# Performance work log

Hardware: AMD Instinct MI355X
Metric: run time of the kernel (lower is better)

The kernel has to match this reference:

```python
import jax, jax.numpy as jnp
import numpy as np
from jax import lax

EPS = 1e-5

def _bn(x, g, b, m, v):
    # eval-mode BatchNorm2d over channel dim of NCHW
    return (x - m[None, :, None, None]) * (g / jnp.sqrt(v + EPS))[None, :, None, None] + b[None, :, None, None]


def _forward(x, proj_w, proj_b, bn0_g, bn0_b, bn0_m, bn0_v,
             in_proj_w, conv_w, conv_b, x_proj_w, dt_w, dt_b, A_log, D,
             out_proj_w, fc_w, fc_b,
             c1_w, c1_b, bn1_g, bn1_b, bn1_m, bn1_v,
             c2_w, c2_b, bn2_g, bn2_b, bn2_m, bn2_v):
    d_state = A_log.shape[1]
    # ---- spectral projection: 1x1 conv + BN + ReLU ----
    p = jnp.einsum('bchw,dc->bdhw', x, proj_w) + proj_b[None, :, None, None]
    p = jax.nn.relu(_bn(p, bn0_g, bn0_b, bn0_m, bn0_v))
    b, d, h, w = p.shape
    L = h * w
    tok = p.reshape(b, d, L).transpose(0, 2, 1)            # [b, L, d_model]

    # ---- Mamba block (d_model=32, d_state=16, d_conv=4, expand=2) ----
    xz = tok @ in_proj_w.T                                 # [b, L, 2*d_in]
    d_in = xz.shape[-1] // 2
    xm, z = xz[..., :d_in], xz[..., d_in:]
    # causal depthwise conv1d along sequence
    xc = lax.conv_general_dilated(
        xm.transpose(0, 2, 1), conv_w[:, None, :], (1,),
        [(conv_w.shape[-1] - 1, 0)], feature_group_count=d_in,
        dimension_numbers=('NCH', 'OIH', 'NCH'))
    u = jax.nn.silu(xc + conv_b[None, :, None]).transpose(0, 2, 1)  # [b, L, d_in]
    xdbl = u @ x_proj_w.T                                  # [b, L, dt_rank+2N]
    dt_rank = dt_w.shape[1]
    dt = xdbl[..., :dt_rank]
    Bm = xdbl[..., dt_rank:dt_rank + d_state]              # [b, L, N]
    Cm = xdbl[..., dt_rank + d_state:]                     # [b, L, N]
    delta = jax.nn.softplus(dt @ dt_w.T + dt_b)            # [b, L, d_in]
    A = -jnp.exp(A_log)                                    # [d_in, N]

    def step(hst, inp):
        d_t, B_t, C_t, u_t = inp                           # [b,d_in],[b,N],[b,N],[b,d_in]
        dA = jnp.exp(d_t[..., None] * A)                   # [b, d_in, N]
        hst = dA * hst + (d_t * u_t)[..., None] * B_t[:, None, :]
        y_t = jnp.einsum('bdn,bn->bd', hst, C_t)
        return hst, y_t

    h0 = jnp.zeros((b, d_in, d_state), dtype=u.dtype)
    xs = (delta.transpose(1, 0, 2), Bm.transpose(1, 0, 2),
          Cm.transpose(1, 0, 2), u.transpose(1, 0, 2))
    _, ys = lax.scan(step, h0, xs)                         # [L, b, d_in]
    y = ys.transpose(1, 0, 2) + u * D                      # D skip
    y = y * jax.nn.silu(z)                                 # gated
    m_out = y @ out_proj_w.T                               # [b, L, d_model]
    mamba_feat = (m_out @ fc_w.T + fc_b).mean(axis=1)      # [b, FEATURE_DIM]

    # ---- CNN branch ----
    dn = ('NCHW', 'OIHW', 'NCHW')
    c = lax.conv_general_dilated(p, c1_w, (1, 1), 'VALID', dimension_numbers=dn) + c1_b[None, :, None, None]
    c = jax.nn.relu(_bn(c, bn1_g, bn1_b, bn1_m, bn1_v))
    c = lax.conv_general_dilated(c, c2_w, (1, 1), 'VALID', dimension_numbers=dn) + c2_b[None, :, None, None]
    c = jax.nn.relu(_bn(c, bn2_g, bn2_b, bn2_m, bn2_v))
    cnn_feat = c.mean(axis=(2, 3))                         # AdaptiveAvgPool2d(1)+Flatten
    return mamba_feat + cnn_feat


def setup_inputs() -> dict:
    key = jax.random.key(0)
    ks = jax.random.split(key, 16)
    B, C_IN, P = 128, 200, 32
    D_MODEL, D_IN, N, DTR, FDIM = 32, 64, 16, 2, 128
    r = lambda k, s, sc=0.05: jax.random.normal(k, s, jnp.float32) * sc
    f32 = jnp.float32
    return {
        'x': jax.random.normal(ks[0], (B, C_IN, P, P), f32),
        'proj_w': r(ks[1], (D_MODEL, C_IN)),
        'proj_b': jnp.zeros((D_MODEL,), f32),
        'bn0_g': jnp.ones((D_MODEL,), f32), 'bn0_b': jnp.zeros((D_MODEL,), f32),
        'bn0_m': jnp.zeros((D_MODEL,), f32), 'bn0_v': jnp.ones((D_MODEL,), f32),
        'in_proj_w': r(ks[2], (2 * D_IN, D_MODEL)),
        'conv_w': r(ks[3], (D_IN, 4), 0.3),
        'conv_b': jnp.zeros((D_IN,), f32),
        'x_proj_w': r(ks[4], (DTR + 2 * N, D_IN)),
        'dt_w': r(ks[5], (D_IN, DTR), 0.5),
        'dt_b': r(ks[6], (D_IN,), 0.5) - 4.0,
        'A_log': jnp.tile(jnp.log(jnp.arange(1, N + 1, dtype=f32))[None, :], (D_IN, 1)),
        'D': jnp.ones((D_IN,), f32),
        'out_proj_w': r(ks[7], (D_MODEL, D_IN)),
        'fc_w': r(ks[8], (FDIM, D_MODEL)),
        'fc_b': jnp.zeros((FDIM,), f32),
        'c1_w': r(ks[9], (32, D_MODEL, 3, 3)),
        'c1_b': jnp.zeros((32,), f32),
        'bn1_g': jnp.ones((32,), f32), 'bn1_b': jnp.zeros((32,), f32),
        'bn1_m': jnp.zeros((32,), f32), 'bn1_v': jnp.ones((32,), f32),
        'c2_w': r(ks[10], (FDIM, 32, 3, 3)),
        'c2_b': jnp.zeros((FDIM,), f32),
        'bn2_g': jnp.ones((FDIM,), f32), 'bn2_b': jnp.zeros((FDIM,), f32),
        'bn2_m': jnp.zeros((FDIM,), f32), 'bn2_v': jnp.ones((FDIM,), f32),
    }


def reference(x, proj_w, proj_b, bn0_g, bn0_b, bn0_m, bn0_v,
              in_proj_w, conv_w, conv_b, x_proj_w, dt_w, dt_b, A_log, D,
              out_proj_w, fc_w, fc_b,
              c1_w, c1_b, bn1_g, bn1_b, bn1_m, bn1_v,
              c2_w, c2_b, bn2_g, bn2_b, bn2_m, bn2_v):
    return _forward(x, proj_w, proj_b, bn0_g, bn0_b, bn0_m, bn0_v,
                    in_proj_w, conv_w, conv_b, x_proj_w, dt_w, dt_b, A_log, D,
                    out_proj_w, fc_w, fc_b,
                    c1_w, c1_b, bn1_g, bn1_b, bn1_m, bn1_v,
                    c2_w, c2_b, bn2_g, bn2_b, bn2_m, bn2_v)
```

## Files before the change

kernel.cpp:

```cpp
#include <hip/hip_runtime.h>
#include <cstdint>

typedef short bf16x8 __attribute__((ext_vector_type(8)));
typedef float f32x4 __attribute__((ext_vector_type(4)));
#define MFMA16(a, b, c) __builtin_amdgcn_mfma_f32_16x16x32_bf16((a), (b), (c), 0, 0, 0)

static __device__ __forceinline__ float fastrcp(float x) {
  float r;
  asm("v_rcp_f32 %0, %1" : "=v"(r) : "v"(x));
  return r;
}
static __device__ __forceinline__ float fastexp2(float x) {
  float r;
  asm("v_exp_f32 %0, %1" : "=v"(r) : "v"(x));
  return r;
}
static __device__ __forceinline__ float silu_(float x) {
  return x * fastrcp(1.f + __expf(-x));
}
static __device__ __forceinline__ unsigned short f2bf(float f) {
  union { float f; unsigned u; } v; v.f = f;
  unsigned r = v.u + 0x7FFF + ((v.u >> 16) & 1);
  return (unsigned short)(r >> 16);
}
static __device__ __forceinline__ void bf2x(unsigned p, float& lo, float& hi) {
  union { unsigned u; float f; } a, bb;
  a.u = p << 16; bb.u = p & 0xffff0000u;
  lo = a.f; hi = bb.f;
}
static __device__ __forceinline__ float bflo(unsigned short h) {
  union { unsigned u; float f; } a;
  a.u = ((unsigned)h) << 16;
  return a.f;
}

__global__ __launch_bounds__(256, 4) void k_front(
    const float* __restrict__ x, const float* __restrict__ pw,
    const float* __restrict__ pb,
    const float* __restrict__ g0, const float* __restrict__ be0,
    const float* __restrict__ mm0, const float* __restrict__ vv0,
    const float* __restrict__ c1_w, const float* __restrict__ c2_w,
    const float* __restrict__ fc_w, const float* __restrict__ opw,
    const float* __restrict__ in_w, const float* __restrict__ xp_w,
    unsigned short* __restrict__ p_bf,
    unsigned short* __restrict__ Wf1, unsigned short* __restrict__ Wf2,
    unsigned short* __restrict__ Wfin, unsigned short* __restrict__ Wfxp,
    float* __restrict__ W2, float* __restrict__ cnn_sum)
{
  __shared__ __align__(16) char fsm[55296];
  int tid = threadIdx.x;
  if (blockIdx.x >= 512) {
    int i = (blockIdx.x - 512) * 256 + tid;
    if (i < 36864) {
      int j = i & 7, l = (i >> 3) & 63, m = (i >> 9) & 7, t = i >> 12;
      int co = m * 16 + (l & 15), ci = ((l >> 4) << 3) + j;
      Wf2[i] = f2bf(c2_w[(size_t)(co * 32 + ci) * 9 + t]);
    } else if (i < 46080) {
      int ii = i - 36864;
      int j = ii & 7, l = (ii >> 3) & 63, m = (ii >> 9) & 1, t = ii >> 10;
      int co = m * 16 + (l & 15), ci = ((l >> 4) << 3) + j;
      Wf1[ii] = f2bf(c1_w[(size_t)(co * 32 + ci) * 9 + t]);
    } else if (i < 54272) {
      int ii = i - 46080;
      int f = ii >> 6, d2 = ii & 63;
      float a = 0.f;
      #pragma unroll
      for (int dm = 0; dm < 32; dm++) a = fmaf(fc_w[(f << 5) + dm], opw[(dm << 6) + d2], a);
      W2[ii] = a;
    } else if (i < 70656) {
      cnn_sum[i - 54272] = 0.f;
    } else if (i < 74752) {
      int ii = i - 70656;
      int j = ii & 7, l = (ii >> 3) & 63, ot = ii >> 9;
      int o = (ot << 4) + (l & 15), c = ((l >> 4) << 3) + j;
      Wfin[ii] = f2bf(in_w[(o << 5) + c]);
    } else if (i < 77824) {
      int ii = i - 74752;
      int j = ii & 7, l = (ii >> 3) & 63, kh = (ii >> 9) & 1, ot = ii >> 10;
      int jr = (ot << 4) + (l & 15), c = (kh << 5) + ((l >> 4) << 3) + j;
      Wfxp[ii] = (jr < 34) ? f2bf(xp_w[(jr << 6) + c]) : (unsigned short)0;
    }
    return;
  }
  unsigned* xT = (unsigned*)fsm;
  unsigned short* WfpL = (unsigned short*)(fsm + 40960);
  int b = blockIdx.x >> 2, l0 = (blockIdx.x & 3) << 8;
  int lane = tid & 63, w = tid >> 6;
  int li = lane & 15, kg4 = (lane >> 4) << 2;
  for (int i = tid; i < 7168; i += 256) {
    int j = i & 7, l = (i >> 3) & 63, m = (i >> 9) & 1, kt = i >> 10;
    int co = (m << 4) + (l & 15), c = (kt << 5) + ((l >> 4) << 3) + j;
    WfpL[i] = (c < 200) ? f2bf(pw[co * 200 + c]) : (unsigned short)0;
  }
  float scv[2][4], sbv[2][4];
  #pragma unroll
  for (int m = 0; m < 2; m++)
    #pragma unroll
    for (int jj = 0; jj < 4; jj++) {
      int co = m * 16 + ((lane >> 4) << 2) + jj;
      float s = g0[co] * rsqrtf(vv0[co] + 1e-5f);
      scv[m][jj] = s;
      sbv[m][jj] = fmaf(pb[co] - mm0[co], s, be0[co]);
    }
  const float* xb = x + (size_t)b * 200 * 1024 + l0 + tid;
  #pragma unroll
  for (int p = 0; p < 16; p++) {
    float v0 = xb[(2 * p) << 10];
    float v1 = xb[(2 * p + 1) << 10];
    xT[tid * 20 + p] = (unsigned)f2bf(v0) | ((unsigned)f2bf(v1) << 16);
  }
  __syncthreads();
  f32x4 acc[4][2];
  #pragma unroll
  for (int q = 0; q < 4; q++) {
    acc[q][0] = (f32x4){0.f, 0.f, 0.f, 0.f};
    acc[q][1] = (f32x4){0.f, 0.f, 0.f, 0.f};
  }
  int buf = 0;
  for (int kt = 0; kt < 7; kt++) {
    if (kt < 6) {
      const float* xc = xb + (((size_t)(kt + 1)) << 15);
      int cb = (kt + 1) * 32;
      #pragma unroll
      for (int p = 0; p < 16; p++) {
        int c = cb + 2 * p;
        float v0 = (c < 200) ? xc[(2 * p) << 10] : 0.f;
        float v1 = (c + 1 < 200) ? xc[(2 * p + 1) << 10] : 0.f;
        xT[(buf ^ 1) * 5120 + tid * 20 + p] = (unsigned)f2bf(v0) | ((unsigned)f2bf(v1) << 16);
      }
    }
    bf16x8 a0 = *reinterpret_cast<const bf16x8*>(&WfpL[(((kt << 1) + 0) * 64 + lane) << 3]);
    bf16x8 a1 = *reinterpret_cast<const bf16x8*>(&WfpL[(((kt << 1) + 1) * 64 + lane) << 3]);
    #pragma unroll
    for (int q = 0; q < 4; q++) {
      int px = ((w + (q << 2)) << 4) + li;
      bf16x8 bfr = *reinterpret_cast<const bf16x8*>(&xT[buf * 5120 + px * 20 + kg4]);
      acc[q][0] = MFMA16(a0, bfr, acc[q][0]);
      acc[q][1] = MFMA16(a1, bfr, acc[q][1]);
    }
    __syncthreads();
    buf ^= 1;
  }
  #pragma unroll
  for (int q = 0; q < 4; q++) {
    int px = ((w + (q << 2)) << 4) + li;
    size_t obase = (((size_t)b << 10) + l0 + px) << 5;
    #pragma unroll
    for (int m = 0; m < 2; m++) {
      f32x4 av = acc[q][m];
      ushort4 pk;
      pk.x = f2bf(fmaxf(fmaf(av[0], scv[m][0], sbv[m][0]), 0.f));
      pk.y = f2bf(fmaxf(fmaf(av[1], scv[m][1], sbv[m][1]), 0.f));
      pk.z = f2bf(fmaxf(fmaf(av[2], scv[m][2], sbv[m][2]), 0.f));
      pk.w = f2bf(fmaxf(fmaf(av[3], scv[m][3], sbv[m][3]), 0.f));
      *reinterpret_cast<ushort4*>(&p_bf[obase + m * 16 + ((lane >> 4) << 2)]) = pk;
    }
  }
}

__global__ __launch_bounds__(1024, 4) void k_mamba(
    const unsigned short* __restrict__ p_bf,
    const unsigned short* __restrict__ Wfin,
    const unsigned short* __restrict__ Wfxp,
    const float* __restrict__ conv_w,
    const float* __restrict__ conv_b,
    const float* __restrict__ dt_w,
    const float* __restrict__ dt_b,
    const float* __restrict__ A_log,
    float* __restrict__ pqrs,
    float* __restrict__ au_g)
{
  __shared__ __align__(16) char smem[65072];
  float* xm  = (float*)smem;
  float* dlS = (float*)smem;
  unsigned short* ubS  = (unsigned short*)(smem + 18224);
  unsigned short* uTb  = (unsigned short*)(smem + 27440);
  unsigned short* duzP = (unsigned short*)(smem + 36656);
  float* bcT  = (float*)(smem + 54064);
  float* cwS  = (float*)(smem + 62768);
  float* cbS  = (float*)(smem + 63792);
  float* dtwS = (float*)(smem + 64048);
  float* dtbS = (float*)(smem + 64560);
  float* auS  = (float*)(smem + 64816);

  int b = blockIdx.x >> 4, ch = blockIdx.x & 15;
  int tid = threadIdx.x, lane = tid & 63, w = tid >> 6;
  int li = lane & 15, cig8 = (lane >> 4) << 3;

  if (tid < 256) cwS[tid] = conv_w[tid];
  else if (tid < 320) cbS[tid - 256] = conv_b[tid - 256];
  else if (tid < 448) dtwS[tid - 320] = dt_w[tid - 320];
  else if (tid < 512) dtbS[tid - 448] = dt_b[tid - 448];
  else if (tid < 576) auS[tid - 512] = 0.f;

  const unsigned short* pbf_b = p_bf + ((size_t)b << 15);

  for (int j = w; j < 36; j += 16) {
    if (j < 20) {
      int ot = j / 5, tt = j % 5;
      int r = tt * 16 + li;
      int tg = (ch << 6) + r - 3;
      bf16x8 bfr = {0,0,0,0,0,0,0,0};
      if (r < 67 && tg >= 0)
        bfr = *reinterpret_cast<const bf16x8*>(pbf_b + ((size_t)tg << 5) + cig8);
      bf16x8 aW = *reinterpret_cast<const bf16x8*>(&Wfin[((ot << 6) + lane) << 3]);
      f32x4 acc = {0.f, 0.f, 0.f, 0.f};
      acc = MFMA16(aW, bfr, acc);
      if (r < 67)
        *reinterpret_cast<float4*>(&xm[r * 68 + (ot << 4) + ((lane >> 4) << 2)]) =
            make_float4(acc[0], acc[1], acc[2], acc[3]);
    } else {
      int jz = j - 20;
      int zot = jz >> 2, tt = jz & 3;
      int t = tt * 16 + li;
      int tg = (ch << 6) + t;
      bf16x8 bfr = *reinterpret_cast<const bf16x8*>(pbf_b + ((size_t)tg << 5) + cig8);
      bf16x8 aW = *reinterpret_cast<const bf16x8*>(&Wfin[(((4 + zot) << 6) + lane) << 3]);
      f32x4 acc = {0.f, 0.f, 0.f, 0.f};
      acc = MFMA16(aW, bfr, acc);
      int dzb = (zot << 4) + ((lane >> 4) << 2);
      int toff = ((t >> 2) << 3) + 4 + (t & 3);
      #pragma unroll
      for (int q = 0; q < 4; q++)
        duzP[(dzb + q) * 136 + toff] = f2bf(silu_(acc[q]));
    }
  }
  __syncthreads();
  {
    int d2 = tid & 63, oct = tid >> 6;
    int t0 = oct << 2;
    float4 cw4 = *reinterpret_cast<const float4*>(&cwS[d2 << 2]);
    float cb1 = cbS[d2];
    float x0 = xm[t0 * 68 + d2], x1 = xm[(t0 + 1) * 68 + d2], x2 = xm[(t0 + 2) * 68 + d2];
    uint2 zz2 = *reinterpret_cast<const uint2*>(&duzP[d2 * 136 + (oct << 3) + 4]);
    float zf[4];
    bf2x(zz2.x, zf[0], zf[1]); bf2x(zz2.y, zf[2], zf[3]);
    unsigned short up[4];
    float aup = 0.f;
    #pragma unroll
    for (int s = 0; s < 4; s++) {
      int t = t0 + s;
      float x3 = xm[(t + 3) * 68 + d2];
      float a = cb1;
      a = fmaf(cw4.x, x0, a); a = fmaf(cw4.y, x1, a);
      a = fmaf(cw4.z, x2, a); a = fmaf(cw4.w, x3, a);
      float uu = silu_(a);
      unsigned short ub_ = f2bf(uu);
      ubS[t * 72 + d2] = ub_;
      up[s] = ub_;
      aup = fmaf(uu, zf[s], aup);
      x0 = x1; x1 = x2; x2 = x3;
    }
    uint2 pk;
    pk.x = (unsigned)up[0] | ((unsigned)up[1] << 16);
    pk.y = (unsigned)up[2] | ((unsigned)up[3] << 16);
    *reinterpret_cast<uint2*>(&uTb[d2 * 72 + t0]) = pk;
    atomicAdd(&auS[d2], aup);
  }
  __syncthreads();
  if (w < 12) {
    int ot = w >> 2, tt = w & 3;
    int t = tt * 16 + li;
    const unsigned short* ub = &ubS[t * 72];
    bf16x8 b0 = *reinterpret_cast<const bf16x8*>(ub + cig8);
    bf16x8 b1 = *reinterpret_cast<const bf16x8*>(ub + 32 + cig8);
    bf16x8 a0 = *reinterpret_cast<const bf16x8*>(&Wfxp[(((ot << 1) + 0) * 64 + lane) << 3]);
    bf16x8 a1 = *reinterpret_cast<const bf16x8*>(&Wfxp[(((ot << 1) + 1) * 64 + lane) << 3]);
    f32x4 acc = {0.f, 0.f, 0.f, 0.f};
    acc = MFMA16(a0, b0, acc);
    acc = MFMA16(a1, b1, acc);
    int jb = (ot << 4) + ((lane >> 4) << 2);
    #pragma unroll
    for (int q = 0; q < 4; q++) {
      int jj = jb + q;
      if (jj < 2) bcT[(t & 31) * 68 + 64 + (jj << 1) + (t >> 5)] = acc[q];
      else if (jj < 34) bcT[(jj - 2) * 68 + t] = acc[q];
    }
  }
  __syncthreads();
  {
    int t = tid >> 4, dq = (tid & 15) << 2;
    int tr = t & 31, th = t >> 5;
    float d0 = bcT[tr * 68 + 64 + th];
    float d1 = bcT[tr * 68 + 66 + th];
    int toff = ((t >> 2) << 3) + (t & 3);
    #pragma unroll
    for (int q = 0; q < 4; q++) {
      int dg = dq + q;
      float pre = fmaf(d0, dtwS[dg << 1], fmaf(d1, dtwS[(dg << 1) + 1], dtbS[dg]));
      float dl_ = (pre > 20.f) ? pre : __logf(1.f + __expf(pre));
      dlS[dg * 68 + t] = dl_;
      float uf = bflo(uTb[dg * 72 + t]);
      duzP[dg * 136 + toff] = f2bf(dl_ * uf);
    }
  }
  __syncthreads();
  {
    int sd = tid >> 4, sn = tid & 15;
    float Areg2 = -__expf(A_log[(sd << 4) + sn]) * 1.44269504f;
    float P = 1.f, qq = 0.f, R = 0.f, S = 0.f;
    const float* dr = &dlS[sd * 68];
    const unsigned short* dz = &duzP[sd * 136];
    const float* Br = &bcT[sn * 68];
    const float* Cr = &bcT[(16 + sn) * 68];
    float4 dv = *reinterpret_cast<const float4*>(dr);
    uint4 duz = *reinterpret_cast<const uint4*>(dz);
    float4 Bv = *reinterpret_cast<const float4*>(Br);
    float4 Cv = *reinterpret_cast<const float4*>(Cr);
    for (int g = 0; g < 16; g++) {
      float4 dvc = dv; uint4 dzc = duz; float4 Bvc = Bv; float4 Cvc = Cv;
      if (g < 15) {
        dv  = *reinterpret_cast<const float4*>(dr + ((g + 1) << 2));
        duz = *reinterpret_cast<const uint4*>(dz + ((g + 1) << 3));
        Bv  = *reinterpret_cast<const float4*>(Br + ((g + 1) << 2));
        Cv  = *reinterpret_cast<const float4*>(Cr + ((g + 1) << 2));
      }
      float du0, du1, du2, du3, z0, z1, z2, z3;
      bf2x(dzc.x, du0, du1); bf2x(dzc.y, du2, du3);
      bf2x(dzc.z, z0, z1);  bf2x(dzc.w, z2, z3);
      float e0 = fastexp2(dvc.x * Areg2), e1 = fastexp2(dvc.y * Areg2);
      float e2 = fastexp2(dvc.z * Areg2), e3 = fastexp2(dvc.w * Areg2);
      float c0 = Cvc.x * z0, c1 = Cvc.y * z1, c2 = Cvc.z * z2, c3 = Cvc.w * z3;
      P = e0 * P; qq = fmaf(e0, qq, du0 * Bvc.x); R = fmaf(c0, P, R); S = fmaf(c0, qq, S);
      P = e1 * P; qq = fmaf(e1, qq, du1 * Bvc.y); R = fmaf(c1, P, R); S = fmaf(c1, qq, S);
      P = e2 * P; qq = fmaf(e2, qq, du2 * Bvc.z); R = fmaf(c2, P, R); S = fmaf(c2, qq, S);
      P = e3 * P; qq = fmaf(e3, qq, du3 * Bvc.w); R = fmaf(c3, P, R); S = fmaf(c3, qq, S);
    }
    size_t idx = ((((size_t)b << 4) + ch) << 10) + (sd << 4) + sn;
    *reinterpret_cast<float4*>(pqrs + (idx << 2)) = make_float4(P, qq, R, S);
    if (sn == 0) au_g[((((size_t)b << 4) + ch) << 6) + sd] = auS[sd];
  }
}

__global__ __launch_bounds__(256) void k_conv1m(
    const unsigned short* __restrict__ p_bf, const unsigned short* __restrict__ Wf1,
    const float* __restrict__ cbias,
    const float* __restrict__ g, const float* __restrict__ be,
    const float* __restrict__ mm, const float* __restrict__ vv,
    unsigned short* __restrict__ c1_bf)
{
  __shared__ __align__(16) unsigned short inS[8 * 32 * 40];
  int b = blockIdx.x / 5, s = blockIdx.x % 5;
  int y0 = s * 6;
  int tid = threadIdx.x, lane = tid & 63, w = tid >> 6;
  int li = lane & 15, cig8 = (lane >> 4) << 3;
  for (int uu = tid; uu < 1024; uu += 256) {
    int r = uu >> 7, rem = uu & 127;
    uint4 v = *reinterpret_cast<const uint4*>(
        &p_bf[((((size_t)b << 10) + (y0 + r) * 32) << 5) + rem * 8]);
    int xx = rem >> 2, cg = rem & 3;
    *reinterpret_cast<uint4*>(&inS[(r * 32 + xx) * 40 + cg * 8]) = v;
  }
  bf16x8 aw[9][2];
  #pragma unroll
  for (int t = 0; t < 9; t++)
    #pragma unroll
    for (int m = 0; m < 2; m++)
      aw[t][m] = *reinterpret_cast<const bf16x8*>(&Wf1[(((t << 1) + m) * 64 + lane) * 8]);
  float scv[2][4], sbv[2][4];
  #pragma unroll
  for (int m = 0; m < 2; m++)
    #pragma unroll
    for (int j = 0; j < 4; j++) {
      int co = m * 16 + ((lane >> 4) << 2) + j;
      float sc = g[co] * rsqrtf(vv[co] + 1e-5f);
      scv[m][j] = sc;
      sbv[m][j] = fmaf(cbias[co] - mm[co], sc, be[co]);
    }
  __syncthreads();
  #pragma unroll
  for (int q = 0; q < 3; q++) {
    int pf = w + q * 4;
    int p = pf * 16 + li;
    int pv = (p < 180) ? p : 0;
    int ry = pv / 30, rx = pv % 30;
    f32x4 a0 = {0.f, 0.f, 0.f, 0.f}, a1 = {0.f, 0.f, 0.f, 0.f};
    #pragma unroll
    for (int t = 0; t < 9; t++) {
      int dy = t / 3, dx = t % 3;
      bf16x8 bfr = *reinterpret_cast<const bf16x8*>(
          &inS[((ry + dy) * 32 + rx + dx) * 40 + cig8]);
      a0 = MFMA16(aw[t][0], bfr, a0);
      a1 = MFMA16(aw[t][1], bfr, a1);
    }
    if (p < 180) {
      size_t obase = ((size_t)b * 900 + (size_t)(y0 + ry) * 30 + rx) << 5;
      #pragma unroll
      for (int m = 0; m < 2; m++) {
        f32x4 av = m ? a1 : a0;
        ushort4 pk;
        pk.x = f2bf(fmaxf(fmaf(av[0], scv[m][0], sbv[m][0]), 0.f));
        pk.y = f2bf(fmaxf(fmaf(av[1], scv[m][1], sbv[m][1]), 0.f));
        pk.z = f2bf(fmaxf(fmaf(av[2], scv[m][2], sbv[m][2]), 0.f));
        pk.w = f2bf(fmaxf(fmaf(av[3], scv[m][3], sbv[m][3]), 0.f));
        *reinterpret_cast<ushort4*>(&c1_bf[obase + m * 16 + ((lane >> 4) << 2)]) = pk;
      }
    }
  }
}

__global__ __launch_bounds__(256) void k_back(
    const unsigned short* __restrict__ c1_bf, const unsigned short* __restrict__ Wf2,
    const float* __restrict__ cb2,
    const float* __restrict__ g, const float* __restrict__ be,
    const float* __restrict__ mm, const float* __restrict__ vv,
    const float* __restrict__ pqrs, const float* __restrict__ au_g,
    const float* __restrict__ Dp,
    float* __restrict__ cnn_sum, float* __restrict__ ybar)
{
  __shared__ __align__(16) unsigned short inS[6 * 30 * 40];
  int tid = threadIdx.x;
  if (blockIdx.x >= 896) {
    int cb = blockIdx.x - 896;
    int b = cb >> 2, qq4 = cb & 3;
    int sd = (qq4 << 4) + (tid >> 4), sn = tid & 15;
    float4 pq[16];
    #pragma unroll
    for (int c = 0; c < 16; c++) {
      size_t idx = ((((size_t)b << 4) + c) << 10) + (sd << 4) + sn;
      pq[c] = *reinterpret_cast<const float4*>(pqrs + (idx << 2));
    }
    float h = 0.f, y = 0.f;
    #pragma unroll
    for (int c = 0; c < 16; c++) {
      y = fmaf(pq[c].z, h, y + pq[c].w);
      h = fmaf(pq[c].x, h, pq[c].y);
    }
    float val = y + Dp[sd] * au_g[((((size_t)b << 4) + sn) << 6) + sd];
    val += __shfl_xor(val, 1); val += __shfl_xor(val, 2);
    val += __shfl_xor(val, 4); val += __shfl_xor(val, 8);
    if (sn == 0) ybar[(b << 6) + sd] = val * (1.f / 1024.f);
    return;
  }
  int b = blockIdx.x / 7, s = blockIdx.x % 7;
  int y0 = s * 4;
  int lane = tid & 63, w = tid >> 6;
  int li = lane & 15, cig8 = (lane >> 4) << 3;
  for (int uu = tid; uu < 720; uu += 256) {
    int r = uu / 120, rem = uu % 120;
    uint4 v = *reinterpret_cast<const uint4*>(
        &c1_bf[(((size_t)b * 900 + (size_t)(y0 + r) * 30) << 5) + rem * 8]);
    int xx = rem >> 2, cg = rem & 3;
    *reinterpret_cast<uint4*>(&inS[(r * 30 + xx) * 40 + cg * 8]) = v;
  }
  bf16x8 aw[9][2];
  #pragma unroll
  for (int t = 0; t < 9; t++)
    #pragma unroll
    for (int m = 0; m < 2; m++)
      aw[t][m] = *reinterpret_cast<const bf16x8*>(&Wf2[(((t << 3) + (w << 1) + m) * 64 + lane) * 8]);
  float scv[2][4], sbv[2][4];
  float psum[2][4] = {{0.f,0.f,0.f,0.f},{0.f,0.f,0.f,0.f}};
  #pragma unroll
  for (int m = 0; m < 2; m++)
    #pragma unroll
    for (int j = 0; j < 4; j++) {
      int co = (w << 5) + m * 16 + ((lane >> 4) << 2) + j;
      float sc = g[co] * rsqrtf(vv[co] + 1e-5f);
      scv[m][j] = sc;
      sbv[m][j] = fmaf(cb2[co] - mm[co], sc, be[co]);
    }
  __syncthreads();
  #pragma unroll
  for (int pf = 0; pf < 7; pf++) {
    int p = pf * 16 + li;
    int ry = p / 28, rx = p % 28;
    f32x4 a0 = {0.f, 0.f, 0.f, 0.f}, a1 = {0.f, 0.f, 0.f, 0.f};
    #pragma unroll
    for (int t = 0; t < 9; t++) {
      int dy = t / 3, dx = t % 3;
      bf16x8 bfr = *reinterpret_cast<const bf16x8*>(
          &inS[((ry + dy) * 30 + rx + dx) * 40 + cig8]);
      a0 = MFMA16(aw[t][0], bfr, a0);
      a1 = MFMA16(aw[t][1], bfr, a1);
    }
    #pragma unroll
    for (int j = 0; j < 4; j++) {
      psum[0][j] += fmaxf(fmaf(a0[j], scv[0][j], sbv[0][j]), 0.f);
      psum[1][j] += fmaxf(fmaf(a1[j], scv[1][j], sbv[1][j]), 0.f);
    }
  }
  #pragma unroll
  for (int m = 0; m < 2; m++)
    #pragma unroll
    for (int j = 0; j < 4; j++) {
      float v = psum[m][j];
      v += __shfl_xor(v, 1); v += __shfl_xor(v, 2);
      v += __shfl_xor(v, 4); v += __shfl_xor(v, 8);
      if (li == 0) {
        int co = (w << 5) + m * 16 + ((lane >> 4) << 2) + j;
        atomicAdd(&cnn_sum[((size_t)b << 7) + co], v);
      }
    }
}

__global__ __launch_bounds__(256) void k_final(
    const float* __restrict__ ybar, const float* __restrict__ W2,
    const float* __restrict__ fc_b, const float* __restrict__ cnn_sum,
    float* __restrict__ out)
{
  int i = blockIdx.x * 256 + threadIdx.x;
  int b = i >> 7, f = i & 127;
  float a = 0.f;
  #pragma unroll
  for (int d2 = 0; d2 < 64; d2++) a = fmaf(ybar[(b << 6) + d2], W2[(f << 6) + d2], a);
  out[i] = a + fc_b[f] + cnn_sum[i] * (1.f / 784.f);
}

extern "C" void kernel_launch(void* const* d_in, const int* in_sizes, int n_in,
                              void* d_out, int out_size, void* d_ws, size_t ws_size,
                              hipStream_t stream) {
  (void)in_sizes; (void)n_in; (void)out_size; (void)ws_size;
  const float* x         = (const float*)d_in[0];
  const float* proj_w    = (const float*)d_in[1];
  const float* proj_b    = (const float*)d_in[2];
  const float* bn0_g     = (const float*)d_in[3];
  const float* bn0_b     = (const float*)d_in[4];
  const float* bn0_m     = (const float*)d_in[5];
  const float* bn0_v     = (const float*)d_in[6];
  const float* in_proj_w = (const float*)d_in[7];
  const float* conv_w    = (const float*)d_in[8];
  const float* conv_b    = (const float*)d_in[9];
  const float* x_proj_w  = (const float*)d_in[10];
  const float* dt_w      = (const float*)d_in[11];
  const float* dt_b      = (const float*)d_in[12];
  const float* A_log     = (const float*)d_in[13];
  const float* Dp        = (const float*)d_in[14];
  const float* out_proj_w= (const float*)d_in[15];
  const float* fc_w      = (const float*)d_in[16];
  const float* fc_b      = (const float*)d_in[17];
  const float* c1_w      = (const float*)d_in[18];
  const float* c1_b      = (const float*)d_in[19];
  const float* bn1_g     = (const float*)d_in[20];
  const float* bn1_b     = (const float*)d_in[21];
  const float* bn1_m     = (const float*)d_in[22];
  const float* bn1_v     = (const float*)d_in[23];
  const float* c2_w      = (const float*)d_in[24];
  const float* c2_b      = (const float*)d_in[25];
  const float* bn2_g     = (const float*)d_in[26];
  const float* bn2_b     = (const float*)d_in[27];
  const float* bn2_m     = (const float*)d_in[28];
  const float* bn2_v     = (const float*)d_in[29];
  float* out = (float*)d_out;
  float* ws  = (float*)d_ws;
  float* ybar    = ws;
  float* cnn_sum = ws + 8192;
  float* W2      = ws + 24576;
  float* pqrs    = ws + 32768;
  float* au_g    = ws + 8421376;
  unsigned short* p_bf  = (unsigned short*)(ws + 8552448);
  unsigned short* c1_bf = (unsigned short*)(ws + 10649600);
  unsigned short* Wf1   = (unsigned short*)(ws + 12492800);
  unsigned short* Wf2   = (unsigned short*)(ws + 12497408);
  unsigned short* Wfin  = (unsigned short*)(ws + 12515840);
  unsigned short* Wfxp  = (unsigned short*)(ws + 12517888);

  k_front<<<dim3(816), dim3(256), 0, stream>>>(x, proj_w, proj_b, bn0_g, bn0_b, bn0_m, bn0_v,
                                               c1_w, c2_w, fc_w, out_proj_w, in_proj_w, x_proj_w,
                                               p_bf, Wf1, Wf2, Wfin, Wfxp, W2, cnn_sum);
  k_mamba<<<dim3(2048), dim3(1024), 0, stream>>>(p_bf, Wfin, Wfxp, conv_w, conv_b, dt_w, dt_b,
                                                 A_log, pqrs, au_g);
  k_conv1m<<<dim3(640), dim3(256), 0, stream>>>(p_bf, Wf1, c1_b, bn1_g, bn1_b, bn1_m, bn1_v, c1_bf);
  k_back<<<dim3(1408), dim3(256), 0, stream>>>(c1_bf, Wf2, c2_b, bn2_g, bn2_b, bn2_m, bn2_v,
                                               pqrs, au_g, Dp, cnn_sum, ybar);
  k_final<<<dim3(64), dim3(256), 0, stream>>>(ybar, W2, fc_b, cnn_sum, out);
}
```

Before: 129.8 us.

## Fold conv1 into mamba launch and restructure conv2 to per-wave global loads

Removes the separate conv1 kernel by giving its work to the first 160 blocks of the mamba launch, where each wave computes a slice directly from global memory without LDS staging. The conv2 part of k_back is regrouped into 1024-thread blocks, with each wave loading inputs and weights from global or cache instead of staging through shared memory and registers. The scan loop drops its manual register prefetch, and the dt/softplus thread mapping changes. Launch bounds go up to 8 waves per SIMD, which may force register spills. Without LDS reuse, conv loads are repeated per tap, and the conv1 blocks hold the full 65 KB shared allocation even though they do not use it.

```diff
diff --git a/kernel.cpp b/kernel.cpp
--- a/kernel.cpp
+++ b/kernel.cpp
@@ -158,7 +158,7 @@
   }
 }
 
-__global__ __launch_bounds__(1024, 4) void k_mamba(
+__global__ __launch_bounds__(1024, 8) void k_mamba(
     const unsigned short* __restrict__ p_bf,
     const unsigned short* __restrict__ Wfin,
     const unsigned short* __restrict__ Wfxp,
@@ -167,10 +167,67 @@
     const float* __restrict__ dt_w,
     const float* __restrict__ dt_b,
     const float* __restrict__ A_log,
+    const unsigned short* __restrict__ Wf1,
+    const float* __restrict__ c1bias,
+    const float* __restrict__ g1, const float* __restrict__ be1,
+    const float* __restrict__ mm1, const float* __restrict__ vv1,
+    unsigned short* __restrict__ c1_bf,
     float* __restrict__ pqrs,
     float* __restrict__ au_g)
 {
   __shared__ __align__(16) char smem[65072];
+  int tid = threadIdx.x, lane = tid & 63, w = tid >> 6;
+  int li = lane & 15, cig8 = (lane >> 4) << 3;
+
+  if (blockIdx.x < 160) {
+    int j = blockIdx.x * 16 + w;
+    int ob = j >> 2, ow = j & 3;
+    int b1 = ob / 5, s1 = ob % 5;
+    int y0 = s1 * 6;
+    float scv[2][4], sbv[2][4];
+    #pragma unroll
+    for (int m = 0; m < 2; m++)
+      #pragma unroll
+      for (int jj = 0; jj < 4; jj++) {
+        int co = m * 16 + ((lane >> 4) << 2) + jj;
+        float sc = g1[co] * rsqrtf(vv1[co] + 1e-5f);
+        scv[m][jj] = sc;
+        sbv[m][jj] = fmaf(c1bias[co] - mm1[co], sc, be1[co]);
+      }
+    #pragma unroll
+    for (int q = 0; q < 3; q++) {
+      int pf = ow + (q << 2);
+      int p = pf * 16 + li;
+      int pv = (p < 180) ? p : 0;
+      int ry = pv / 30, rx = pv % 30;
+      f32x4 a0 = {0.f, 0.f, 0.f, 0.f}, a1 = {0.f, 0.f, 0.f, 0.f};
+      #pragma unroll
+      for (int t = 0; t < 9; t++) {
+        int dy = t / 3, dx = t % 3;
+        bf16x8 bfr = *reinterpret_cast<const bf16x8*>(
+            &p_bf[((((size_t)b1 << 10) + (y0 + ry + dy) * 32 + rx + dx) << 5) + cig8]);
+        bf16x8 w0 = *reinterpret_cast<const bf16x8*>(&Wf1[(((t << 1) + 0) * 64 + lane) << 3]);
+        bf16x8 w1 = *reinterpret_cast<const bf16x8*>(&Wf1[(((t << 1) + 1) * 64 + lane) << 3]);
+        a0 = MFMA16(w0, bfr, a0);
+        a1 = MFMA16(w1, bfr, a1);
+      }
+      if (p < 180) {
+        size_t obase = ((size_t)b1 * 900 + (size_t)(y0 + ry) * 30 + rx) << 5;
+        #pragma unroll
+        for (int m = 0; m < 2; m++) {
+          f32x4 av = m ? a1 : a0;
+          ushort4 pk;
+          pk.x = f2bf(fmaxf(fmaf(av[0], scv[m][0], sbv[m][0]), 0.f));
+          pk.y = f2bf(fmaxf(fmaf(av[1], scv[m][1], sbv[m][1]), 0.f));
+          pk.z = f2bf(fmaxf(fmaf(av[2], scv[m][2], sbv[m][2]), 0.f));
+          pk.w = f2bf(fmaxf(fmaf(av[3], scv[m][3], sbv[m][3]), 0.f));
+          *reinterpret_cast<ushort4*>(&c1_bf[obase + m * 16 + ((lane >> 4) << 2)]) = pk;
+        }
+      }
+    }
+    return;
+  }
+
   float* xm  = (float*)smem;
   float* dlS = (float*)smem;
   unsigned short* ubS  = (unsigned short*)(smem + 18224);
@@ -183,9 +240,8 @@
   float* dtbS = (float*)(smem + 64560);
   float* auS  = (float*)(smem + 64816);
 
-  int b = blockIdx.x >> 4, ch = blockIdx.x & 15;
-  int tid = threadIdx.x, lane = tid & 63, w = tid >> 6;
-  int li = lane & 15, cig8 = (lane >> 4) << 3;
+  int bm = blockIdx.x - 160;
+  int b = bm >> 4, ch = bm & 15;
 
   if (tid < 256) cwS[tid] = conv_w[tid];
   else if (tid < 320) cbS[tid - 256] = conv_b[tid - 256];
@@ -279,14 +335,14 @@
   }
   __syncthreads();
   {
-    int t = tid >> 4, dq = (tid & 15) << 2;
+    int t = tid >> 4, l15 = tid & 15;
     int tr = t & 31, th = t >> 5;
     float d0 = bcT[tr * 68 + 64 + th];
     float d1 = bcT[tr * 68 + 66 + th];
     int toff = ((t >> 2) << 3) + (t & 3);
     #pragma unroll
     for (int q = 0; q < 4; q++) {
-      int dg = dq + q;
+      int dg = l15 + (q << 4);
       float pre = fmaf(d0, dtwS[dg << 1], fmaf(d1, dtwS[(dg << 1) + 1], dtbS[dg]));
       float dl_ = (pre > 20.f) ? pre : __logf(1.f + __expf(pre));
       dlS[dg * 68 + t] = dl_;
@@ -303,28 +359,21 @@
     const unsigned short* dz = &duzP[sd * 136];
     const float* Br = &bcT[sn * 68];
     const float* Cr = &bcT[(16 + sn) * 68];
-    float4 dv = *reinterpret_cast<const float4*>(dr);
-    uint4 duz = *reinterpret_cast<const uint4*>(dz);
-    float4 Bv = *reinterpret_cast<const float4*>(Br);
-    float4 Cv = *reinterpret_cast<const float4*>(Cr);
     for (int g = 0; g < 16; g++) {
-      float4 dvc = dv; uint4 dzc = duz; float4 Bvc = Bv; float4 Cvc = Cv;
-      if (g < 15) {
-        dv  = *reinterpret_cast<const float4*>(dr + ((g + 1) << 2));
-        duz = *reinterpret_cast<const uint4*>(dz + ((g + 1) << 3));
-        Bv  = *reinterpret_cast<const float4*>(Br + ((g + 1) << 2));
-        Cv  = *reinterpret_cast<const float4*>(Cr + ((g + 1) << 2));
-      }
+      float4 dv = *reinterpret_cast<const float4*>(dr + (g << 2));
+      uint4 duz = *reinterpret_cast<const uint4*>(dz + (g << 3));
+      float4 Bv = *reinterpret_cast<const float4*>(Br + (g << 2));
+      float4 Cv = *reinterpret_cast<const float4*>(Cr + (g << 2));
       float du0, du1, du2, du3, z0, z1, z2, z3;
-      bf2x(dzc.x, du0, du1); bf2x(dzc.y, du2, du3);
-      bf2x(dzc.z, z0, z1);  bf2x(dzc.w, z2, z3);
-      float e0 = fastexp2(dvc.x * Areg2), e1 = fastexp2(dvc.y * Areg2);
-      float e2 = fastexp2(dvc.z * Areg2), e3 = fastexp2(dvc.w * Areg2);
-      float c0 = Cvc.x * z0, c1 = Cvc.y * z1, c2 = Cvc.z * z2, c3 = Cvc.w * z3;
-      P = e0 * P; qq = fmaf(e0, qq, du0 * Bvc.x); R = fmaf(c0, P, R); S = fmaf(c0, qq, S);
-      P = e1 * P; qq = fmaf(e1, qq, du1 * Bvc.y); R = fmaf(c1, P, R); S = fmaf(c1, qq, S);
-      P = e2 * P; qq = fmaf(e2, qq, du2 * Bvc.z); R = fmaf(c2, P, R); S = fmaf(c2, qq, S);
-      P = e3 * P; qq = fmaf(e3, qq, du3 * Bvc.w); R = fmaf(c3, P, R); S = fmaf(c3, qq, S);
+      bf2x(duz.x, du0, du1); bf2x(duz.y, du2, du3);
+      bf2x(duz.z, z0, z1);  bf2x(duz.w, z2, z3);
+      float e0 = fastexp2(dv.x * Areg2), e1 = fastexp2(dv.y * Areg2);
+      float e2 = fastexp2(dv.z * Areg2), e3 = fastexp2(dv.w * Areg2);
+      float c0 = Cv.x * z0, c1 = Cv.y * z1, c2 = Cv.z * z2, c3 = Cv.w * z3;
+      P = e0 * P; qq = fmaf(e0, qq, du0 * Bv.x); R = fmaf(c0, P, R); S = fmaf(c0, qq, S);
+      P = e1 * P; qq = fmaf(e1, qq, du1 * Bv.y); R = fmaf(c1, P, R); S = fmaf(c1, qq, S);
+      P = e2 * P; qq = fmaf(e2, qq, du2 * Bv.z); R = fmaf(c2, P, R); S = fmaf(c2, qq, S);
+      P = e3 * P; qq = fmaf(e3, qq, du3 * Bv.w); R = fmaf(c3, P, R); S = fmaf(c3, qq, S);
     }
     size_t idx = ((((size_t)b << 4) + ch) << 10) + (sd << 4) + sn;
     *reinterpret_cast<float4*>(pqrs + (idx << 2)) = make_float4(P, qq, R, S);
@@ -332,74 +381,7 @@
   }
 }
 
-__global__ __launch_bounds__(256) void k_conv1m(
-    const unsigned short* __restrict__ p_bf, const unsigned short* __restrict__ Wf1,
-    const float* __restrict__ cbias,
-    const float* __restrict__ g, const float* __restrict__ be,
-    const float* __restrict__ mm, const float* __restrict__ vv,
-    unsigned short* __restrict__ c1_bf)
-{
-  __shared__ __align__(16) unsigned short inS[8 * 32 * 40];
-  int b = blockIdx.x / 5, s = blockIdx.x % 5;
-  int y0 = s * 6;
-  int tid = threadIdx.x, lane = tid & 63, w = tid >> 6;
-  int li = lane & 15, cig8 = (lane >> 4) << 3;
-  for (int uu = tid; uu < 1024; uu += 256) {
-    int r = uu >> 7, rem = uu & 127;
-    uint4 v = *reinterpret_cast<const uint4*>(
-        &p_bf[((((size_t)b << 10) + (y0 + r) * 32) << 5) + rem * 8]);
-    int xx = rem >> 2, cg = rem & 3;
-    *reinterpret_cast<uint4*>(&inS[(r * 32 + xx) * 40 + cg * 8]) = v;
-  }
-  bf16x8 aw[9][2];
-  #pragma unroll
-  for (int t = 0; t < 9; t++)
-    #pragma unroll
-    for (int m = 0; m < 2; m++)
-      aw[t][m] = *reinterpret_cast<const bf16x8*>(&Wf1[(((t << 1) + m) * 64 + lane) * 8]);
-  float scv[2][4], sbv[2][4];
-  #pragma unroll
-  for (int m = 0; m < 2; m++)
-    #pragma unroll
-    for (int j = 0; j < 4; j++) {
-      int co = m * 16 + ((lane >> 4) << 2) + j;
-      float sc = g[co] * rsqrtf(vv[co] + 1e-5f);
-      scv[m][j] = sc;
-      sbv[m][j] = fmaf(cbias[co] - mm[co], sc, be[co]);
-    }
-  __syncthreads();
-  #pragma unroll
-  for (int q = 0; q < 3; q++) {
-    int pf = w + q * 4;
-    int p = pf * 16 + li;
-    int pv = (p < 180) ? p : 0;
-    int ry = pv / 30, rx = pv % 30;
-    f32x4 a0 = {0.f, 0.f, 0.f, 0.f}, a1 = {0.f, 0.f, 0.f, 0.f};
-    #pragma unroll
-    for (int t = 0; t < 9; t++) {
-      int dy = t / 3, dx = t % 3;
-      bf16x8 bfr = *reinterpret_cast<const bf16x8*>(
-          &inS[((ry + dy) * 32 + rx + dx) * 40 + cig8]);
-      a0 = MFMA16(aw[t][0], bfr, a0);
-      a1 = MFMA16(aw[t][1], bfr, a1);
-    }
-    if (p < 180) {
-      size_t obase = ((size_t)b * 900 + (size_t)(y0 + ry) * 30 + rx) << 5;
-      #pragma unroll
-      for (int m = 0; m < 2; m++) {
-        f32x4 av = m ? a1 : a0;
-        ushort4 pk;
-        pk.x = f2bf(fmaxf(fmaf(av[0], scv[m][0], sbv[m][0]), 0.f));
-        pk.y = f2bf(fmaxf(fmaf(av[1], scv[m][1], sbv[m][1]), 0.f));
-        pk.z = f2bf(fmaxf(fmaf(av[2], scv[m][2], sbv[m][2]), 0.f));
-        pk.w = f2bf(fmaxf(fmaf(av[3], scv[m][3], sbv[m][3]), 0.f));
-        *reinterpret_cast<ushort4*>(&c1_bf[obase + m * 16 + ((lane >> 4) << 2)]) = pk;
-      }
-    }
-  }
-}
-
-__global__ __launch_bounds__(256) void k_back(
+__global__ __launch_bounds__(1024, 8) void k_back(
     const unsigned short* __restrict__ c1_bf, const unsigned short* __restrict__ Wf2,
     const float* __restrict__ cb2,
     const float* __restrict__ g, const float* __restrict__ be,
@@ -408,23 +390,24 @@
     const float* __restrict__ Dp,
     float* __restrict__ cnn_sum, float* __restrict__ ybar)
 {
-  __shared__ __align__(16) unsigned short inS[6 * 30 * 40];
-  int tid = threadIdx.x;
-  if (blockIdx.x >= 896) {
-    int cb = blockIdx.x - 896;
-    int b = cb >> 2, qq4 = cb & 3;
-    int sd = (qq4 << 4) + (tid >> 4), sn = tid & 15;
-    float4 pq[16];
-    #pragma unroll
-    for (int c = 0; c < 16; c++) {
-      size_t idx = ((((size_t)b << 4) + c) << 10) + (sd << 4) + sn;
-      pq[c] = *reinterpret_cast<const float4*>(pqrs + (idx << 2));
-    }
+  int tid = threadIdx.x, lane = tid & 63, w = tid >> 6;
+  int li = lane & 15, cig8 = (lane >> 4) << 3;
+  if (blockIdx.x >= 224) {
+    int b = blockIdx.x - 224;
+    int sd = tid >> 4, sn = tid & 15;
     float h = 0.f, y = 0.f;
-    #pragma unroll
-    for (int c = 0; c < 16; c++) {
-      y = fmaf(pq[c].z, h, y + pq[c].w);
-      h = fmaf(pq[c].x, h, pq[c].y);
+    for (int half = 0; half < 2; half++) {
+      float4 pq[8];
+      #pragma unroll
+      for (int c = 0; c < 8; c++) {
+        size_t idx = ((((size_t)b << 4) + (half << 3) + c) << 10) + (sd << 4) + sn;
+        pq[c] = *reinterpret_cast<const float4*>(pqrs + (idx << 2));
+      }
+      #pragma unroll
+      for (int c = 0; c < 8; c++) {
+        y = fmaf(pq[c].z, h, y + pq[c].w);
+        h = fmaf(pq[c].x, h, pq[c].y);
+      }
     }
     float val = y + Dp[sd] * au_g[((((size_t)b << 4) + sn) << 6) + sd];
     val += __shfl_xor(val, 1); val += __shfl_xor(val, 2);
@@ -432,35 +415,21 @@
     if (sn == 0) ybar[(b << 6) + sd] = val * (1.f / 1024.f);
     return;
   }
-  int b = blockIdx.x / 7, s = blockIdx.x % 7;
+  int j = blockIdx.x * 16 + w;
+  int ob = j >> 2, ow = j & 3;
+  int b = ob / 7, s = ob % 7;
   int y0 = s * 4;
-  int lane = tid & 63, w = tid >> 6;
-  int li = lane & 15, cig8 = (lane >> 4) << 3;
-  for (int uu = tid; uu < 720; uu += 256) {
-    int r = uu / 120, rem = uu % 120;
-    uint4 v = *reinterpret_cast<const uint4*>(
-        &c1_bf[(((size_t)b * 900 + (size_t)(y0 + r) * 30) << 5) + rem * 8]);
-    int xx = rem >> 2, cg = rem & 3;
-    *reinterpret_cast<uint4*>(&inS[(r * 30 + xx) * 40 + cg * 8]) = v;
-  }
-  bf16x8 aw[9][2];
-  #pragma unroll
-  for (int t = 0; t < 9; t++)
-    #pragma unroll
-    for (int m = 0; m < 2; m++)
-      aw[t][m] = *reinterpret_cast<const bf16x8*>(&Wf2[(((t << 3) + (w << 1) + m) * 64 + lane) * 8]);
   float scv[2][4], sbv[2][4];
   float psum[2][4] = {{0.f,0.f,0.f,0.f},{0.f,0.f,0.f,0.f}};
   #pragma unroll
   for (int m = 0; m < 2; m++)
     #pragma unroll
-    for (int j = 0; j < 4; j++) {
-      int co = (w << 5) + m * 16 + ((lane >> 4) << 2) + j;
+    for (int jj = 0; jj < 4; jj++) {
+      int co = (ow << 5) + m * 16 + ((lane >> 4) << 2) + jj;
       float sc = g[co] * rsqrtf(vv[co] + 1e-5f);
-      scv[m][j] = sc;
-      sbv[m][j] = fmaf(cb2[co] - mm[co], sc, be[co]);
-    }
-  __syncthreads();
+      scv[m][jj] = sc;
+      sbv[m][jj] = fmaf(cb2[co] - mm[co], sc, be[co]);
+    }
   #pragma unroll
   for (int pf = 0; pf < 7; pf++) {
     int p = pf * 16 + li;
@@ -470,25 +439,27 @@
     for (int t = 0; t < 9; t++) {
       int dy = t / 3, dx = t % 3;
       bf16x8 bfr = *reinterpret_cast<const bf16x8*>(
-          &inS[((ry + dy) * 30 + rx + dx) * 40 + cig8]);
-      a0 = MFMA16(aw[t][0], bfr, a0);
-      a1 = MFMA16(aw[t][1], bfr, a1);
-    }
-    #pragma unroll
-    for (int j = 0; j < 4; j++) {
-      psum[0][j] += fmaxf(fmaf(a0[j], scv[0][j], sbv[0][j]), 0.f);
-      psum[1][j] += fmaxf(fmaf(a1[j], scv[1][j], sbv[1][j]), 0.f);
+          &c1_bf[(((size_t)b * 900 + (size_t)(y0 + ry + dy) * 30 + rx + dx) << 5) + cig8]);
+      bf16x8 w0 = *reinterpret_cast<const bf16x8*>(&Wf2[(((t << 3) + (ow << 1) + 0) * 64 + lane) << 3]);
+      bf16x8 w1 = *reinterpret_cast<const bf16x8*>(&Wf2[(((t << 3) + (ow << 1) + 1) * 64 + lane) << 3]);
+      a0 = MFMA16(w0, bfr, a0);
+      a1 = MFMA16(w1, bfr, a1);
+    }
+    #pragma unroll
+    for (int jj = 0; jj < 4; jj++) {
+      psum[0][jj] += fmaxf(fmaf(a0[jj], scv[0][jj], sbv[0][jj]), 0.f);
+      psum[1][jj] += fmaxf(fmaf(a1[jj], scv[1][jj], sbv[1][jj]), 0.f);
     }
   }
   #pragma unroll
   for (int m = 0; m < 2; m++)
     #pragma unroll
-    for (int j = 0; j < 4; j++) {
-      float v = psum[m][j];
+    for (int jj = 0; jj < 4; jj++) {
+      float v = psum[m][jj];
       v += __shfl_xor(v, 1); v += __shfl_xor(v, 2);
       v += __shfl_xor(v, 4); v += __shfl_xor(v, 8);
       if (li == 0) {
-        int co = (w << 5) + m * 16 + ((lane >> 4) << 2) + j;
+        int co = (ow << 5) + m * 16 + ((lane >> 4) << 2) + jj;
         atomicAdd(&cnn_sum[((size_t)b << 7) + co], v);
       }
     }
@@ -558,10 +529,10 @@
   k_front<<<dim3(816), dim3(256), 0, stream>>>(x, proj_w, proj_b, bn0_g, bn0_b, bn0_m, bn0_v,
                                                c1_w, c2_w, fc_w, out_proj_w, in_proj_w, x_proj_w,
                                                p_bf, Wf1, Wf2, Wfin, Wfxp, W2, cnn_sum);
-  k_mamba<<<dim3(2048), dim3(1024), 0, stream>>>(p_bf, Wfin, Wfxp, conv_w, conv_b, dt_w, dt_b,
-                                                 A_log, pqrs, au_g);
-  k_conv1m<<<dim3(640), dim3(256), 0, stream>>>(p_bf, Wf1, c1_b, bn1_g, bn1_b, bn1_m, bn1_v, c1_bf);
-  k_back<<<dim3(1408), dim3(256), 0, stream>>>(c1_bf, Wf2, c2_b, bn2_g, bn2_b, bn2_m, bn2_v,
+  k_mamba<<<dim3(2208), dim3(1024), 0, stream>>>(p_bf, Wfin, Wfxp, conv_w, conv_b, dt_w, dt_b,
+                                                 A_log, Wf1, c1_b, bn1_g, bn1_b, bn1_m, bn1_v,
+                                                 c1_bf, pqrs, au_g);
+  k_back<<<dim3(352), dim3(1024), 0, stream>>>(c1_bf, Wf2, c2_b, bn2_g, bn2_b, bn2_m, bn2_v,
                                                pqrs, au_g, Dp, cnn_sum, ybar);
   k_final<<<dim3(64), dim3(256), 0, stream>>>(ybar, W2, fc_b, cnn_sum, out);
 }
```

Measured after the change: 258.3 us. 99.0% more time.
